# Performance work log

Measured on AMD Instinct MI355X. Metric: run time of the kernel, lower is better.

The kernel has to match this reference:

```python
import jax, jax.numpy as jnp
import numpy as np

D = 256
H1, H2 = 256, 128

def setup_inputs() -> dict:
    key0 = jax.random.key(0)
    ks = jax.random.split(key0, 10)
    B, Lq, Lk = 2, 512, 512
    query = jax.random.normal(ks[0], (B, Lq, D), dtype=jnp.float32)
    key_t = jax.random.normal(ks[1], (B, Lk, D), dtype=jnp.float32)
    value = jax.random.normal(ks[2], (B, Lk, D), dtype=jnp.float32)
    mask = jnp.ones((B, Lq, Lk), dtype=jnp.int32)
    s1 = 1.0 / np.sqrt(2 * D)
    W1 = jax.random.uniform(ks[3], (2 * D, H1), jnp.float32, -s1, s1)  # torch Linear(2D,H1), [in,out]
    b1 = jax.random.uniform(ks[4], (H1,), jnp.float32, -s1, s1)
    s2 = 1.0 / np.sqrt(H1)
    W2 = jax.random.uniform(ks[5], (H1, H2), jnp.float32, -s2, s2)
    b2 = jax.random.uniform(ks[6], (H2,), jnp.float32, -s2, s2)
    s3 = 1.0 / np.sqrt(H2)
    W3 = jax.random.uniform(ks[7], (H2, 1), jnp.float32, -s3, s3)
    b3 = jax.random.uniform(ks[8], (1,), jnp.float32, -s3, s3)
    return {"query": query, "key": key_t, "value": value, "mask": mask,
            "W1": W1, "b1": b1, "W2": W2, "b2": b2, "W3": W3, "b3": b3}

def reference(query, key, value, mask, W1, b1, W2, b2, W3, b3):
    # Original: cat([q_i, k_j]) @ W1 == q_i @ W1[:D] + k_j @ W1[D:]  (algebraic split,
    # identical math, avoids materializing the [B,Lq,Lk,2D] concat tensor).
    W1q, W1k = W1[:D], W1[D:]
    qp = jnp.einsum('bqd,dh->bqh', query, W1q)           # [B,Lq,H1]
    kp = jnp.einsum('bkd,dh->bkh', key, W1k)             # [B,Lk,H1]
    h1 = jax.nn.relu(qp[:, :, None, :] + kp[:, None, :, :] + b1)   # [B,Lq,Lk,H1]
    h2 = jax.nn.relu(jnp.einsum('bqkh,hj->bqkj', h1, W2) + b2)      # [B,Lq,Lk,H2]
    scores = (jnp.einsum('bqkj,jo->bqko', h2, W3) + b3)[..., 0]     # [B,Lq,Lk]
    scores = jnp.where(mask == 0, jnp.float32(-1e9), scores)
    attn = jax.nn.softmax(scores, axis=-1)               # dropout is identity in eval mode
    out = jnp.einsum('bqk,bkd->bqd', attn, value)
    return out, attn
```

## Files before the change

kernel.cpp:

```cpp
#include <hip/hip_runtime.h>

#define D_  256
#define H1_ 256
#define H2_ 128
#define B_  2
#define LQ_ 512
#define LK_ 512
#define BK  64

typedef float  f32x4  __attribute__((ext_vector_type(4)));
typedef __bf16 bf16x8 __attribute__((ext_vector_type(8)));
typedef __bf16 bf16x4 __attribute__((ext_vector_type(4)));

__global__ __launch_bounds__(512) void prep_kernel(
    const float* __restrict__ query, const float* __restrict__ key,
    const float* __restrict__ W1, const float* __restrict__ b1,
    const float* __restrict__ W2,
    float* __restrict__ qp, float* __restrict__ kp, __bf16* __restrict__ w2f) {
  const int blk = blockIdx.x;
  const int tid = threadIdx.x;
  if (blk >= 512) {
    const int id   = (blk - 512) * 512 + tid;
    const int j    = id & 7;
    const int lane = (id >> 3) & 63;
    const int frag = id >> 9;
    const int nt = frag & 3;
    const int wn = (frag >> 2) & 1;
    const int ks = (frag >> 3) & 1;
    const int kc = frag >> 4;
    const int n = wn * 64 + nt * 16 + (lane & 15);
    const int k = kc * 64 + ks * 32 + ((lane >> 4) << 3) + j;
    w2f[id] = (__bf16)W2[k * H2_ + n];
    return;
  }
  __shared__ float in_lds[4][D_];
  __shared__ float part[4][H1_];
  const int row0 = blk * 4;
  const int sel  = row0 >> 10;
  const float* __restrict__ src = sel ? key : query;
  const int base = (row0 & 1023) * D_;
  for (int i = tid; i < 4 * D_; i += 512)
    in_lds[i >> 8][i & 255] = src[base + i];
  __syncthreads();
  const int h  = tid & 255;
  const int kh = tid >> 8;
  float acc[4] = {0.f, 0.f, 0.f, 0.f};
  const float* __restrict__ w = W1 + sel * D_ * H1_ + kh * 128 * H1_ + h;
#pragma unroll 4
  for (int dd = 0; dd < 128; ++dd) {
    const float wv = w[dd * H1_];
    const int d = kh * 128 + dd;
#pragma unroll
    for (int r = 0; r < 4; ++r) acc[r] += in_lds[r][d] * wv;
  }
  if (kh == 1) {
#pragma unroll
    for (int r = 0; r < 4; ++r) part[r][h] = acc[r];
  }
  __syncthreads();
  if (kh == 0) {
    const float bias = sel ? 0.0f : b1[h];
    float* __restrict__ dst = sel ? kp : qp;
#pragma unroll
    for (int r = 0; r < 4; ++r)
      dst[base + r * H1_ + h] = acc[r] + part[r][h] + bias;
  }
}

__global__ __launch_bounds__(256, 2) void score_kernel(
    const float* __restrict__ qp, const float* __restrict__ kp,
    const __bf16* __restrict__ w2f,
    const float* __restrict__ b2, const float* __restrict__ W3,
    const float* __restrict__ b3, float* __restrict__ scores) {
  __shared__ __align__(16) __bf16 A_lds[128 * BK];
  __shared__ float  spart[2][128];

  const int b  = blockIdx.z;
  const int q0 = blockIdx.y * 8;
  const int k0 = blockIdx.x * 16;
  const int tid  = threadIdx.x;
  const int wave = tid >> 6;
  const int lane = tid & 63;
  const int quad = lane >> 4;
  const int l16  = lane & 15;
  const int wm   = wave >> 1;
  const int wn   = wave & 1;
  const int h8   = l16 & 7;

  const int qi = tid >> 5;
  const int t5 = (tid >> 4) & 1;
  const int kg = tid & 15;

  const float* __restrict__ qpb = qp + (b * LQ_ + q0) * H1_;
  const float* __restrict__ kpb = kp + (b * LK_ + k0) * H1_;

  f32x4 acc[4][4];
#pragma unroll
  for (int mt = 0; mt < 4; ++mt)
#pragma unroll
    for (int nt = 0; nt < 4; ++nt)
      acc[mt][nt] = (f32x4){0.f, 0.f, 0.f, 0.f};

  for (int kc = 0; kc < H1_ / BK; ++kc) {
    bf16x8 bfr[2][4];
#pragma unroll
    for (int ks = 0; ks < 2; ++ks)
#pragma unroll
      for (int nt = 0; nt < 4; ++nt)
        bfr[ks][nt] = *(const bf16x8*)(
            w2f + ((((kc * 2 + ks) * 2 + wn) * 4 + nt) * 64 + lane) * 8);

    const float4 qv = *(const float4*)(qpb + qi * H1_ + kc * BK + kg * 4);
#pragma unroll
    for (int ii = 0; ii < 8; ++ii) {
      const int ki = t5 * 8 + ii;
      const int r  = qi * 16 + ki;
      const float4 kv = *(const float4*)(kpb + ki * H1_ + kc * BK + kg * 4);
      bf16x4 a;
      a[0] = (__bf16)fmaxf(qv.x + kv.x, 0.f);
      a[1] = (__bf16)fmaxf(qv.y + kv.y, 0.f);
      a[2] = (__bf16)fmaxf(qv.z + kv.z, 0.f);
      a[3] = (__bf16)fmaxf(qv.w + kv.w, 0.f);
      const int sw = (((kg >> 1) ^ (r & 7)) << 3) + ((kg & 1) << 2);
      *(bf16x4*)(&A_lds[r * BK + sw]) = a;
    }
    __syncthreads();
#pragma unroll
    for (int ks = 0; ks < 2; ++ks) {
      const int cbase = ks * 4 + quad;
      bf16x8 af[4];
#pragma unroll
      for (int mt = 0; mt < 4; ++mt) {
        const int ra = wm * 64 + mt * 16 + l16;
        af[mt] = *(const bf16x8*)(&A_lds[ra * BK + ((cbase ^ h8) << 3)]);
      }
#pragma unroll
      for (int mt = 0; mt < 4; ++mt)
#pragma unroll
        for (int nt = 0; nt < 4; ++nt)
          acc[mt][nt] = __builtin_amdgcn_mfma_f32_16x16x32_bf16(
              af[mt], bfr[ks][nt], acc[mt][nt], 0, 0, 0);
    }
    __syncthreads();
  }

  float part[4][4];
#pragma unroll
  for (int mt = 0; mt < 4; ++mt)
#pragma unroll
    for (int rg = 0; rg < 4; ++rg) part[mt][rg] = 0.f;
#pragma unroll
  for (int nt = 0; nt < 4; ++nt) {
    const int col = wn * 64 + nt * 16 + l16;
    const float b2v = b2[col];
    const float w3v = W3[col];
#pragma unroll
    for (int mt = 0; mt < 4; ++mt)
#pragma unroll
      for (int rg = 0; rg < 4; ++rg) {
        float h2 = acc[mt][nt][rg] + b2v;
        h2 = fmaxf(h2, 0.f);
        part[mt][rg] += h2 * w3v;
      }
  }
#pragma unroll
  for (int off = 1; off < 16; off <<= 1)
#pragma unroll
    for (int mt = 0; mt < 4; ++mt)
#pragma unroll
      for (int rg = 0; rg < 4; ++rg)
        part[mt][rg] += __shfl_xor(part[mt][rg], off, 64);
  if (l16 == 0) {
#pragma unroll
    for (int mt = 0; mt < 4; ++mt)
#pragma unroll
      for (int rg = 0; rg < 4; ++rg) {
        const int rl = wm * 64 + mt * 16 + quad * 4 + rg;
        spart[wn][rl] = part[mt][rg];
      }
  }
  __syncthreads();
  if (tid < 128) {
    const float s = spart[0][tid] + spart[1][tid] + b3[0];
    const int qi2 = tid >> 4, ki2 = tid & 15;
    scores[(b * LQ_ + q0 + qi2) * LK_ + k0 + ki2] = s;
  }
}

__global__ __launch_bounds__(512) void smout_kernel(
    const float* __restrict__ sc, float* __restrict__ attn,
    const int* __restrict__ mask, const float* __restrict__ value,
    float* __restrict__ out) {
  const int ds = blockIdx.x, qg = blockIdx.y, b = blockIdx.z;
  const int tid = threadIdx.x;
  __shared__ float a_lds[8][LK_];
  __shared__ float p_lds[3][8][128];
  const int row0 = b * LQ_ + qg * 8;
  const int w = tid >> 6, lane = tid & 63;
  {
    const float* __restrict__ srow = sc + (row0 + w) * LK_;
    const int*  __restrict__ mrow = mask + (row0 + w) * LK_;
    float v[8];
#pragma unroll
    for (int j = 0; j < 8; ++j) {
      float s = srow[lane + j * 64];
      if (mrow[lane + j * 64] == 0) s = -1e9f;
      v[j] = s;
    }
    float m = v[0];
#pragma unroll
    for (int j = 1; j < 8; ++j) m = fmaxf(m, v[j]);
#pragma unroll
    for (int off = 32; off; off >>= 1) m = fmaxf(m, __shfl_xor(m, off, 64));
    float sum = 0.f;
#pragma unroll
    for (int j = 0; j < 8; ++j) { v[j] = __expf(v[j] - m); sum += v[j]; }
#pragma unroll
    for (int off = 32; off; off >>= 1) sum += __shfl_xor(sum, off, 64);
    const float inv = 1.f / sum;
    float* __restrict__ arow = attn + (row0 + w) * LK_;
#pragma unroll
    for (int j = 0; j < 8; ++j) {
      const float p = v[j] * inv;
      a_lds[w][lane + j * 64] = p;
      if (ds == 0) arow[lane + j * 64] = p;
    }
  }
  __syncthreads();
  const int dl = tid & 127;
  const int d  = dl + ds * 128;
  const int kh = tid >> 7;
  float acc[8] = {0.f, 0.f, 0.f, 0.f, 0.f, 0.f, 0.f, 0.f};
  const float* __restrict__ vb = value + (b * LK_ + kh * 128) * D_ + d;
#pragma unroll 4
  for (int k = 0; k < 128; ++k) {
    const float v = vb[k * D_];
    const float* __restrict__ ar = &a_lds[0][kh * 128 + k];
#pragma unroll
    for (int q = 0; q < 8; ++q) acc[q] += ar[q * LK_] * v;
  }
  if (kh > 0) {
#pragma unroll
    for (int q = 0; q < 8; ++q) p_lds[kh - 1][q][dl] = acc[q];
  }
  __syncthreads();
  if (kh == 0) {
    float* __restrict__ ob = out + row0 * D_ + d;
#pragma unroll
    for (int q = 0; q < 8; ++q)
      ob[q * D_] = acc[q] + p_lds[0][q][dl] + p_lds[1][q][dl] + p_lds[2][q][dl];
  }
}

extern "C" void kernel_launch(void* const* d_in, const int* in_sizes, int n_in,
                              void* d_out, int out_size, void* d_ws, size_t ws_size,
                              hipStream_t stream) {
  (void)in_sizes; (void)n_in; (void)out_size; (void)ws_size;
  const float* query = (const float*)d_in[0];
  const float* key   = (const float*)d_in[1];
  const float* value = (const float*)d_in[2];
  const int*   mask  = (const int*)d_in[3];
  const float* W1    = (const float*)d_in[4];
  const float* b1    = (const float*)d_in[5];
  const float* W2    = (const float*)d_in[6];
  const float* b2    = (const float*)d_in[7];
  const float* W3    = (const float*)d_in[8];
  const float* b3    = (const float*)d_in[9];

  float* out  = (float*)d_out;
  float* attn = out + B_ * LQ_ * D_;

  float*  qp  = (float*)d_ws;
  float*  kp  = qp + B_ * LQ_ * H1_;
  __bf16* w2f = (__bf16*)(kp + B_ * LK_ * H1_);
  float*  sc  = (float*)(w2f + H2_ * H1_);

  prep_kernel<<<576, 512, 0, stream>>>(query, key, W1, b1, W2, qp, kp, w2f);
  dim3 gscore(LK_ / 16, LQ_ / 8, B_);
  score_kernel<<<gscore, 256, 0, stream>>>(qp, kp, w2f, b2, W3, b3, sc);
  smout_kernel<<<dim3(2, 64, B_), 512, 0, stream>>>(sc, attn, mask, value, out);
}
```

Before: 147.7 us.

## Restructure softmax-PV kernel: 4 rows per block, full D, float4 value loads

```diff
diff --git a/kernel.cpp b/kernel.cpp
--- a/kernel.cpp
+++ b/kernel.cpp
@@ -191,13 +191,13 @@
     const float* __restrict__ sc, float* __restrict__ attn,
     const int* __restrict__ mask, const float* __restrict__ value,
     float* __restrict__ out) {
-  const int ds = blockIdx.x, qg = blockIdx.y, b = blockIdx.z;
+  const int qg = blockIdx.x, b = blockIdx.y;
   const int tid = threadIdx.x;
-  __shared__ float a_lds[8][LK_];
-  __shared__ float p_lds[3][8][128];
-  const int row0 = b * LQ_ + qg * 8;
+  __shared__ __align__(16) float a_lds[LK_][4];
+  __shared__ __align__(16) f32x4 p_lds[7][4][64];
+  const int row0 = b * LQ_ + qg * 4;
   const int w = tid >> 6, lane = tid & 63;
-  {
+  if (w < 4) {
     const float* __restrict__ srow = sc + (row0 + w) * LK_;
     const int*  __restrict__ mrow = mask + (row0 + w) * LK_;
     float v[8];
@@ -222,33 +222,38 @@
 #pragma unroll
     for (int j = 0; j < 8; ++j) {
       const float p = v[j] * inv;
-      a_lds[w][lane + j * 64] = p;
-      if (ds == 0) arow[lane + j * 64] = p;
-    }
-  }
-  __syncthreads();
-  const int dl = tid & 127;
-  const int d  = dl + ds * 128;
-  const int kh = tid >> 7;
-  float acc[8] = {0.f, 0.f, 0.f, 0.f, 0.f, 0.f, 0.f, 0.f};
-  const float* __restrict__ vb = value + (b * LK_ + kh * 128) * D_ + d;
+      a_lds[lane + j * 64][w] = p;
+      arow[lane + j * 64] = p;
+    }
+  }
+  __syncthreads();
+  const int kh2 = tid >> 6;
+  const int dv  = tid & 63;
+  f32x4 acc[4];
+#pragma unroll
+  for (int q = 0; q < 4; ++q) acc[q] = (f32x4){0.f, 0.f, 0.f, 0.f};
+  const f32x4* __restrict__ vb4 = (const f32x4*)value + (b * LK_ + kh2 * 64) * 64 + dv;
 #pragma unroll 4
-  for (int k = 0; k < 128; ++k) {
-    const float v = vb[k * D_];
-    const float* __restrict__ ar = &a_lds[0][kh * 128 + k];
-#pragma unroll
-    for (int q = 0; q < 8; ++q) acc[q] += ar[q * LK_] * v;
-  }
-  if (kh > 0) {
-#pragma unroll
-    for (int q = 0; q < 8; ++q) p_lds[kh - 1][q][dl] = acc[q];
-  }
-  __syncthreads();
-  if (kh == 0) {
-    float* __restrict__ ob = out + row0 * D_ + d;
-#pragma unroll
-    for (int q = 0; q < 8; ++q)
-      ob[q * D_] = acc[q] + p_lds[0][q][dl] + p_lds[1][q][dl] + p_lds[2][q][dl];
+  for (int k = 0; k < 64; ++k) {
+    const f32x4 v4 = vb4[k * 64];
+    const f32x4 p4 = *(const f32x4*)(&a_lds[kh2 * 64 + k][0]);
+#pragma unroll
+    for (int q = 0; q < 4; ++q) acc[q] += p4[q] * v4;
+  }
+  if (kh2 > 0) {
+#pragma unroll
+    for (int q = 0; q < 4; ++q) p_lds[kh2 - 1][q][dv] = acc[q];
+  }
+  __syncthreads();
+  if (kh2 == 0) {
+    f32x4* __restrict__ ob4 = (f32x4*)out + row0 * 64 + dv;
+#pragma unroll
+    for (int q = 0; q < 4; ++q) {
+      f32x4 r = acc[q];
+#pragma unroll
+      for (int pp = 0; pp < 7; ++pp) r += p_lds[pp][q][dv];
+      ob4[q * 64] = r;
+    }
   }
 }
 
@@ -278,5 +283,5 @@
   prep_kernel<<<576, 512, 0, stream>>>(query, key, W1, b1, W2, qp, kp, w2f);
   dim3 gscore(LK_ / 16, LQ_ / 8, B_);
   score_kernel<<<gscore, 256, 0, stream>>>(qp, kp, w2f, b2, W3, b3, sc);
-  smout_kernel<<<dim3(2, 64, B_), 512, 0, stream>>>(sc, attn, mask, value, out);
-}
+  smout_kernel<<<dim3(128, B_), 512, 0, stream>>>(sc, attn, mask, value, out);
+}
```

Result: faster. 141.1 us (-4.5%).
